# Kernel optimization log

Hardware: AMD Instinct MI355X
Metric: run time of the kernel (lower is better)

Reference implementation:

```python
import jax, jax.numpy as jnp
import numpy as np

EMBED = 1024
HEADS = 16
HEAD_DIM = EMBED // HEADS


def setup_inputs() -> dict:
    key = jax.random.key(0)
    ks = jax.random.split(key, 9)
    s = 0.02
    x = jax.random.normal(ks[0], (2, 2048, EMBED), dtype=jnp.float32)
    Wq = jax.random.normal(ks[1], (EMBED, EMBED), dtype=jnp.float32) * s
    bq = jnp.zeros((EMBED,), dtype=jnp.float32)
    Wk = jax.random.normal(ks[2], (EMBED, EMBED), dtype=jnp.float32) * s
    bk = jnp.zeros((EMBED,), dtype=jnp.float32)
    Wv = jax.random.normal(ks[3], (EMBED, EMBED), dtype=jnp.float32) * s
    bv = jnp.zeros((EMBED,), dtype=jnp.float32)
    Wo = jax.random.normal(ks[4], (EMBED, EMBED), dtype=jnp.float32) * s
    bo = jnp.zeros((EMBED,), dtype=jnp.float32)
    return {"x": x, "Wq": Wq, "bq": bq, "Wk": Wk, "bk": bk,
            "Wv": Wv, "bv": bv, "Wo": Wo, "bo": bo}


def reference(x, Wq, bq, Wk, bk, Wv, bv, Wo, bo):
    B, S, E = x.shape
    H, D = HEADS, HEAD_DIM
    scale = jnp.sqrt(jnp.asarray(D, dtype=x.dtype))
    # projections (torch Linear: y = x @ W.T + b)
    q = (x @ Wq.T + bq).reshape(B, S, H, D).transpose(0, 2, 1, 3)  # [B,H,S,D]
    k = (x @ Wk.T + bk).reshape(B, S, H, D).transpose(0, 2, 1, 3)
    v = (x @ Wv.T + bv).reshape(B, S, H, D).transpose(0, 2, 1, 3)
    scores = jnp.einsum('bhqd,bhkd->bhqk', q, k) / scale  # [B,H,S,S]
    probs = jax.nn.softmax(scores, axis=-1)
    out = jnp.einsum('bhqk,bhkd->bhqd', probs, v)  # [B,H,S,D]
    out = out.transpose(0, 2, 1, 3).reshape(B, S, E)
    return out @ Wo.T + bo
```

## Files before the change

### kernel.cpp

```cpp
#include <hip/hip_runtime.h>
#include <cstddef>

#define EMBED 1024
#define HEADS 16
#define HDIM  64
#define BATCH 2
#define SEQ   2048
#define MTOT  (BATCH*SEQ)

typedef __attribute__((ext_vector_type(8)))  short short8;
typedef __attribute__((ext_vector_type(4)))  float f32x4;
typedef __attribute__((ext_vector_type(16))) float f32x16;

typedef __attribute__((address_space(1))) const unsigned int* gas_u32p;
typedef __attribute__((address_space(3))) unsigned int* las_u32p;

static __device__ __forceinline__ void gload_lds16(const void* g, void* l) {
    __builtin_amdgcn_global_load_lds((gas_u32p)g, (las_u32p)l, 16, 0, 0);
}

static __device__ __forceinline__ unsigned short f2bf(float x) {
    unsigned u = __builtin_bit_cast(unsigned, x);
    unsigned r = (u + 0x7FFFu + ((u >> 16) & 1u)) >> 16;
    return (unsigned short)r;
}

static __device__ __forceinline__ unsigned pk_bf16(float lo, float hi) {
    unsigned r;
    asm("v_cvt_pk_bf16_f32 %0, %1, %2" : "=v"(r) : "v"(lo), "v"(hi));
    return r;
}

static __device__ __forceinline__ void plane32_swap(unsigned &a, unsigned &b) {
    auto r = __builtin_amdgcn_permlane32_swap((int)a, (int)b, false, false);
    a = (unsigned)r[0];
    b = (unsigned)r[1];
}

static __device__ __forceinline__ f32x16 mfma32(short8 a, short8 b, f32x16 c) {
    return __builtin_amdgcn_mfma_f32_32x32x16_bf16(a, b, c, 0, 0, 0);
}

__global__ __launch_bounds__(256)
void convx(const float* __restrict__ x, unsigned short* __restrict__ xh)
{
    const size_t i = ((size_t)blockIdx.x * 256 + threadIdx.x) * 8;
    float4 a = *(const float4*)(x + i);
    float4 b = *(const float4*)(x + i + 4);
    unsigned short o[8] __attribute__((aligned(16)));
    o[0] = f2bf(a.x); o[1] = f2bf(a.y); o[2] = f2bf(a.z); o[3] = f2bf(a.w);
    o[4] = f2bf(b.x); o[5] = f2bf(b.y); o[6] = f2bf(b.z); o[7] = f2bf(b.w);
    *(uint4*)(xh + i) = *(const uint4*)o;
}

__global__ __launch_bounds__(256)
void convw(const float* __restrict__ Wq, const float* __restrict__ Wk,
           const float* __restrict__ Wv, const float* __restrict__ Wo,
           unsigned short* __restrict__ Wh)
{
    const int sel = blockIdx.y;
    const float* src = sel == 0 ? Wq : sel == 1 ? Wk : sel == 2 ? Wv : Wo;
    unsigned short* dst = Wh + (size_t)sel * EMBED * EMBED;
    const size_t i = ((size_t)blockIdx.x * 256 + threadIdx.x) * 4;
    float4 a = *(const float4*)(src + i);
    ushort4 o;
    o.x = f2bf(a.x); o.y = f2bf(a.y); o.z = f2bf(a.z); o.w = f2bf(a.w);
    *(ushort4*)(dst + i) = o;
}

__global__ __launch_bounds__(256)
void gemm_qkv_bf16(const unsigned short* __restrict__ A,
                   const unsigned short* __restrict__ Wqh,
                   const unsigned short* __restrict__ Wkh,
                   const unsigned short* __restrict__ Wvh,
                   const float* __restrict__ bq,
                   const float* __restrict__ bk,
                   const float* __restrict__ bv,
                   unsigned short* __restrict__ Qb,
                   unsigned short* __restrict__ Kb,
                   unsigned short* __restrict__ Vt)
{
    __shared__ short As[128 * 32];
    __shared__ short Bs[128 * 32];

    const int tid  = threadIdx.x;
    const int lane = tid & 63;
    const int w    = tid >> 6;
    const int c    = lane & 15;
    const int g    = lane >> 4;
    const int wr   = w >> 1;
    const int wc   = w & 1;

    const int m0   = blockIdx.y * 128;
    const int bx   = blockIdx.x;
    const int wsel = bx >> 3;
    const int n0   = (bx & 7) * 128;

    const unsigned short* W = (wsel == 0) ? Wqh : (wsel == 1) ? Wkh : Wvh;
    const float* bias       = (wsel == 0) ? bq  : (wsel == 1) ? bk  : bv;

    f32x4 acc[4][4] = {};

    for (int k0 = 0; k0 < EMBED; k0 += 32) {
        __syncthreads();
        #pragma unroll
        for (int i = 0; i < 2; ++i) {
            int s   = (w * 2 + i) * 64 + lane;
            int row = s >> 2;
            int k8  = (s & 3) * 8;
            gload_lds16(A + (size_t)(m0 + row) * EMBED + k0 + k8,
                        As + (size_t)(w * 2 + i) * 512);
            gload_lds16(W + (size_t)(n0 + row) * EMBED + k0 + k8,
                        Bs + (size_t)(w * 2 + i) * 512);
        }
        __syncthreads();

        short8 af[4], bf[4];
        #pragma unroll
        for (int mi = 0; mi < 4; ++mi)
            af[mi] = *(const short8*)&As[(wr * 64 + mi * 16 + c) * 32 + g * 8];
        #pragma unroll
        for (int ni = 0; ni < 4; ++ni)
            bf[ni] = *(const short8*)&Bs[(wc * 64 + ni * 16 + c) * 32 + g * 8];
        #pragma unroll
        for (int mi = 0; mi < 4; ++mi)
            #pragma unroll
            for (int ni = 0; ni < 4; ++ni)
                acc[mi][ni] = __builtin_amdgcn_mfma_f32_16x16x32_bf16(
                    af[mi], bf[ni], acc[mi][ni], 0, 0, 0);
    }

    if (wsel == 2) {
        #pragma unroll
        for (int mi = 0; mi < 4; ++mi) {
            const int m  = m0 + wr * 64 + mi * 16 + g * 4;
            const int bb = m >> 11;
            const int ss = m & (SEQ - 1);
            #pragma unroll
            for (int ni = 0; ni < 4; ++ni) {
                const int col = n0 + wc * 64 + ni * 16 + c;
                const int hh = col >> 6, dd = col & 63;
                const float bi_ = bias[col];
                ushort4 o;
                o.x = f2bf(acc[mi][ni][0] + bi_);
                o.y = f2bf(acc[mi][ni][1] + bi_);
                o.z = f2bf(acc[mi][ni][2] + bi_);
                o.w = f2bf(acc[mi][ni][3] + bi_);
                *(ushort4*)&Vt[((size_t)((bb * HEADS + hh) * HDIM) + dd) * SEQ + ss] = o;
            }
        }
    } else {
        unsigned short* Out = (wsel == 0) ? Qb : Kb;
        const float oscale  = (wsel == 0) ? 0.180336880f : 1.0f;
        #pragma unroll
        for (int mi = 0; mi < 4; ++mi)
            #pragma unroll
            for (int r = 0; r < 4; ++r) {
                const int m = m0 + wr * 64 + mi * 16 + g * 4 + r;
                #pragma unroll
                for (int ni = 0; ni < 4; ++ni) {
                    const int col = n0 + wc * 64 + ni * 16 + c;
                    Out[(size_t)m * EMBED + col] =
                        f2bf((acc[mi][ni][r] + bias[col]) * oscale);
                }
            }
    }
}

__global__ __launch_bounds__(256)
void gemm_o_bf16(const unsigned short* __restrict__ A,
                 const unsigned short* __restrict__ Woh,
                 const float* __restrict__ bo,
                 float* __restrict__ C)
{
    __shared__ short As[128 * 32];
    __shared__ short Bs[128 * 32];

    const int tid  = threadIdx.x;
    const int lane = tid & 63;
    const int w    = tid >> 6;
    const int c    = lane & 15;
    const int g    = lane >> 4;
    const int wr   = w >> 1;
    const int wc   = w & 1;

    const int m0 = blockIdx.y * 128;
    const int n0 = blockIdx.x * 128;

    f32x4 acc[4][4] = {};

    for (int k0 = 0; k0 < EMBED; k0 += 32) {
        __syncthreads();
        #pragma unroll
        for (int i = 0; i < 2; ++i) {
            int s   = (w * 2 + i) * 64 + lane;
            int row = s >> 2;
            int k8  = (s & 3) * 8;
            gload_lds16(A + (size_t)(m0 + row) * EMBED + k0 + k8,
                        As + (size_t)(w * 2 + i) * 512);
            gload_lds16(Woh + (size_t)(n0 + row) * EMBED + k0 + k8,
                        Bs + (size_t)(w * 2 + i) * 512);
        }
        __syncthreads();

        short8 af[4], bf[4];
        #pragma unroll
        for (int mi = 0; mi < 4; ++mi)
            af[mi] = *(const short8*)&As[(wr * 64 + mi * 16 + c) * 32 + g * 8];
        #pragma unroll
        for (int ni = 0; ni < 4; ++ni)
            bf[ni] = *(const short8*)&Bs[(wc * 64 + ni * 16 + c) * 32 + g * 8];
        #pragma unroll
        for (int mi = 0; mi < 4; ++mi)
            #pragma unroll
            for (int ni = 0; ni < 4; ++ni)
                acc[mi][ni] = __builtin_amdgcn_mfma_f32_16x16x32_bf16(
                    af[mi], bf[ni], acc[mi][ni], 0, 0, 0);
    }

    #pragma unroll
    for (int mi = 0; mi < 4; ++mi)
        #pragma unroll
        for (int r = 0; r < 4; ++r) {
            const int m = m0 + wr * 64 + mi * 16 + g * 4 + r;
            #pragma unroll
            for (int ni = 0; ni < 4; ++ni) {
                const int col = n0 + wc * 64 + ni * 16 + c;
                C[(size_t)m * EMBED + col] = acc[mi][ni][r] + bo[col];
            }
        }
}

__global__ __launch_bounds__(512, 4)
void flash_attn_mfma5(const unsigned short* __restrict__ Qb,
                      const unsigned short* __restrict__ Kb,
                      const unsigned short* __restrict__ Vt,
                      unsigned short* __restrict__ O)
{
    __shared__ short KT[2][2][64 * 64];
    __shared__ short VT[2][2][64 * 64];

    const int tid  = threadIdx.x;
    const int lane = tid & 63;
    const int w    = tid >> 6;
    const int qt   = w & 3;
    const int half = w >> 2;
    const int l31  = lane & 31;
    const int hi   = lane >> 5;
    const int q0   = blockIdx.x * 128 + qt * 32;
    const int h    = blockIdx.y;
    const int b    = blockIdx.z;

    short8 qf[4];
    {
        const unsigned short* qrow =
            Qb + (size_t)(b * SEQ + q0 + l31) * EMBED + h * HDIM + hi * 8;
        #pragma unroll
        for (int kc = 0; kc < 4; ++kc)
            qf[kc] = *(const short8*)(qrow + kc * 16);
    }

    const int tb     = w >> 1;
    const int sthalf = tb >> 1;
    const int stV    = tb & 1;
    const int ssub   = w & 1;
    const int strow  = ssub * 32 + (lane >> 3);
    const int ch     = (lane & 7) ^ (strow & 7);
    const unsigned short* kS =
        Kb + (size_t)(b * SEQ + sthalf * (SEQ / 2) + strow) * EMBED + h * HDIM + ch * 8;
    const unsigned short* vS =
        Vt + ((size_t)((b * HEADS + h) * HDIM) + strow) * SEQ + sthalf * (SEQ / 2) + ch * 8;

    f32x16 acc[2] = {};
    float l_run = 0.f;

    #define STAGE(kt2, bb)                                                    \
        do {                                                                  \
            if (stV == 0) {                                                   \
                const unsigned short* src = kS + (size_t)(kt2) * 64 * EMBED;  \
                short* kd = &KT[sthalf][bb][ssub * 2048];                     \
                _Pragma("unroll")                                             \
                for (int it = 0; it < 4; ++it)                                \
                    gload_lds16(src + (size_t)it * 8 * EMBED, kd + it * 512); \
            } else {                                                          \
                const unsigned short* src = vS + (kt2) * 64;                  \
                short* vd = &VT[sthalf][bb][ssub * 2048];                     \
                _Pragma("unroll")                                             \
                for (int it = 0; it < 4; ++it)                                \
                    gload_lds16(src + (size_t)it * 8 * SEQ, vd + it * 512);   \
            }                                                                 \
        } while (0)

    STAGE(0, 0);
    __syncthreads();

    for (int kt = 0; kt < SEQ / 2 / 64; ++kt) {
        const int bi = kt & 1;
        if (kt < SEQ / 2 / 64 - 1) STAGE(kt + 1, bi ^ 1);

        const short* kb_ = &KT[half][bi][0];
        const short* vb_ = &VT[half][bi][0];

        f32x16 s[2] = {};
        __builtin_amdgcn_s_setprio(1);
        #pragma unroll
        for (int t = 0; t < 2; ++t) {
            const int row = t * 32 + l31;
            const int rm  = l31 & 7;
            #pragma unroll
            for (int kc = 0; kc < 4; ++kc) {
                short8 ka = *(const short8*)&kb_[row * 64 + (((2 * kc + hi) ^ rm) * 8)];
                s[t] = mfma32(ka, qf[kc], s[t]);
            }
        }
        __builtin_amdgcn_s_setprio(0);

        float rs = 0.f;
        #pragma unroll
        for (int t = 0; t < 2; ++t)
            #pragma unroll
            for (int r = 0; r < 16; ++r) {
                float pv = __builtin_amdgcn_exp2f(s[t][r]);
                s[t][r] = pv;
                rs += pv;
            }
        rs += __shfl_xor(rs, 32, 64);
        l_run += rs;

        short8 pf[2][2];
        #pragma unroll
        for (int t = 0; t < 2; ++t)
            #pragma unroll
            for (int kc = 0; kc < 2; ++kc) {
                unsigned A0 = pk_bf16(s[t][8 * kc + 0], s[t][8 * kc + 1]);
                unsigned A1 = pk_bf16(s[t][8 * kc + 2], s[t][8 * kc + 3]);
                unsigned B0 = pk_bf16(s[t][8 * kc + 4], s[t][8 * kc + 5]);
                unsigned B1 = pk_bf16(s[t][8 * kc + 6], s[t][8 * kc + 7]);
                plane32_swap(A0, B0);
                plane32_swap(A1, B1);
                uint4 fw = make_uint4(A0, A1, B0, B1);
                pf[t][kc] = __builtin_bit_cast(short8, fw);
            }

        __builtin_amdgcn_s_setprio(1);
        #pragma unroll
        for (int dt = 0; dt < 2; ++dt) {
            const int row = dt * 32 + l31;
            const int rm  = l31 & 7;
            #pragma unroll
            for (int t = 0; t < 2; ++t)
                #pragma unroll
                for (int kc = 0; kc < 2; ++kc) {
                    short8 vf = *(const short8*)
                        &vb_[row * 64 + (((4 * t + 2 * kc + hi) ^ rm) * 8)];
                    acc[dt] = mfma32(pf[t][kc], vf, acc[dt]);
                }
        }
        __builtin_amdgcn_s_setprio(0);

        __syncthreads();
    }
    #undef STAGE

    float* mrgf = (float*)&KT[0][0][0];
    float* mlbf = (float*)&VT[0][0][0];
    if (half == 1) {
        #pragma unroll
        for (int dt = 0; dt < 2; ++dt)
            #pragma unroll
            for (int r = 0; r < 16; ++r) {
                const int qr = (r & 3) + 8 * (r >> 2) + 4 * hi;
                mrgf[qt * 2048 + qr * 64 + dt * 32 + l31] = acc[dt][r];
            }
        if (lane < 32)
            mlbf[qt * 32 + lane] = l_run;
    }
    __syncthreads();
    if (half == 0) {
        const float lo  = mlbf[qt * 32 + l31];
        const float inv = 1.f / (l_run + lo);
        #pragma unroll
        for (int r = 0; r < 16; ++r) {
            const int qr = (r & 3) + 8 * (r >> 2) + 4 * hi;
            float invr = __shfl(inv, qr, 64);
            #pragma unroll
            for (int dt = 0; dt < 2; ++dt) {
                float oh  = mrgf[qt * 2048 + qr * 64 + dt * 32 + l31];
                float val = (acc[dt][r] + oh) * invr;
                O[(size_t)(b * SEQ + q0 + qr) * EMBED + h * HDIM + dt * 32 + l31]
                    = f2bf(val);
            }
        }
    }
}

extern "C" void kernel_launch(void* const* d_in, const int* in_sizes, int n_in,
                              void* d_out, int out_size, void* d_ws, size_t ws_size,
                              hipStream_t stream)
{
    const float* x  = (const float*)d_in[0];
    const float* Wq = (const float*)d_in[1];
    const float* bq = (const float*)d_in[2];
    const float* Wk = (const float*)d_in[3];
    const float* bk = (const float*)d_in[4];
    const float* Wv = (const float*)d_in[5];
    const float* bv = (const float*)d_in[6];
    const float* Wo = (const float*)d_in[7];
    const float* bo = (const float*)d_in[8];
    float* out = (float*)d_out;

    const size_t ME = (size_t)MTOT * EMBED;
    unsigned short* xh   = (unsigned short*)d_ws;
    unsigned short* Qb   = xh   + ME;
    unsigned short* Kb   = Qb   + ME;
    unsigned short* Vt   = Kb   + ME;
    unsigned short* attn = Vt   + ME;
    unsigned short* Wh   = attn + ME;

    dim3 blk(256);

    convx<<<dim3(MTOT * EMBED / 2048), blk, 0, stream>>>(x, xh);
    convw<<<dim3(EMBED * EMBED / 1024, 4), blk, 0, stream>>>(Wq, Wk, Wv, Wo, Wh);

    gemm_qkv_bf16<<<dim3(24, MTOT / 128), blk, 0, stream>>>(
        xh, Wh, Wh + (size_t)EMBED * EMBED, Wh + 2 * (size_t)EMBED * EMBED,
        bq, bk, bv, Qb, Kb, Vt);

    flash_attn_mfma5<<<dim3(SEQ / 128, HEADS, BATCH), dim3(512), 0, stream>>>(
        Qb, Kb, Vt, attn);

    gemm_o_bf16<<<dim3(EMBED / 128, MTOT / 128), blk, 0, stream>>>(
        attn, Wh + 3 * (size_t)EMBED * EMBED, bo, out);
}
```

Baseline: 125.9 us.

## Double-buffer LDS in projection GEMMs and remap blocks for XCD locality

```diff
diff --git a/kernel.cpp b/kernel.cpp
--- a/kernel.cpp
+++ b/kernel.cpp
@@ -80,8 +80,8 @@
                    unsigned short* __restrict__ Kb,
                    unsigned short* __restrict__ Vt)
 {
-    __shared__ short As[128 * 32];
-    __shared__ short Bs[128 * 32];
+    __shared__ short As[2][128 * 32];
+    __shared__ short Bs[2][128 * 32];
 
     const int tid  = threadIdx.x;
     const int lane = tid & 63;
@@ -91,44 +91,61 @@
     const int wr   = w >> 1;
     const int wc   = w & 1;
 
-    const int m0   = blockIdx.y * 128;
-    const int bx   = blockIdx.x;
-    const int wsel = bx >> 3;
-    const int n0   = (bx & 7) * 128;
+    const int lg   = (blockIdx.x & 7) * 96 + (blockIdx.x >> 3);
+    const int m0   = (lg / 24) * 128;
+    const int bxn  = lg % 24;
+    const int wsel = bxn >> 3;
+    const int n0   = (bxn & 7) * 128;
 
     const unsigned short* W = (wsel == 0) ? Wqh : (wsel == 1) ? Wkh : Wvh;
     const float* bias       = (wsel == 0) ? bq  : (wsel == 1) ? bk  : bv;
 
+    const int srow = (w * 2) * 16 + (lane >> 2);
+    const int sk8  = (lane & 3) * 8;
+    const unsigned short* aS0 = A + (size_t)(m0 + srow) * EMBED + sk8;
+    const unsigned short* aS1 = A + (size_t)(m0 + srow + 16) * EMBED + sk8;
+    const unsigned short* bS0 = W + (size_t)(n0 + srow) * EMBED + sk8;
+    const unsigned short* bS1 = W + (size_t)(n0 + srow + 16) * EMBED + sk8;
+    const int d0 = (w * 2) * 512;
+    const int d1 = (w * 2 + 1) * 512;
+
+    #define GSTAGE(bb)                                 \
+        do {                                           \
+            gload_lds16(aS0, &As[bb][d0]);             \
+            gload_lds16(aS1, &As[bb][d1]);             \
+            gload_lds16(bS0, &Bs[bb][d0]);             \
+            gload_lds16(bS1, &Bs[bb][d1]);             \
+            aS0 += 32; aS1 += 32; bS0 += 32; bS1 += 32;\
+        } while (0)
+
     f32x4 acc[4][4] = {};
 
-    for (int k0 = 0; k0 < EMBED; k0 += 32) {
-        __syncthreads();
-        #pragma unroll
-        for (int i = 0; i < 2; ++i) {
-            int s   = (w * 2 + i) * 64 + lane;
-            int row = s >> 2;
-            int k8  = (s & 3) * 8;
-            gload_lds16(A + (size_t)(m0 + row) * EMBED + k0 + k8,
-                        As + (size_t)(w * 2 + i) * 512);
-            gload_lds16(W + (size_t)(n0 + row) * EMBED + k0 + k8,
-                        Bs + (size_t)(w * 2 + i) * 512);
-        }
-        __syncthreads();
+    GSTAGE(0);
+    __syncthreads();
+
+    for (int t = 0; t < EMBED / 32; ++t) {
+        const int cb = t & 1;
+        if (t < EMBED / 32 - 1) GSTAGE(cb ^ 1);
 
         short8 af[4], bf[4];
         #pragma unroll
         for (int mi = 0; mi < 4; ++mi)
-            af[mi] = *(const short8*)&As[(wr * 64 + mi * 16 + c) * 32 + g * 8];
+            af[mi] = *(const short8*)&As[cb][(wr * 64 + mi * 16 + c) * 32 + g * 8];
         #pragma unroll
         for (int ni = 0; ni < 4; ++ni)
-            bf[ni] = *(const short8*)&Bs[(wc * 64 + ni * 16 + c) * 32 + g * 8];
+            bf[ni] = *(const short8*)&Bs[cb][(wc * 64 + ni * 16 + c) * 32 + g * 8];
+        __builtin_amdgcn_s_setprio(1);
         #pragma unroll
         for (int mi = 0; mi < 4; ++mi)
             #pragma unroll
             for (int ni = 0; ni < 4; ++ni)
                 acc[mi][ni] = __builtin_amdgcn_mfma_f32_16x16x32_bf16(
                     af[mi], bf[ni], acc[mi][ni], 0, 0, 0);
-    }
+        __builtin_amdgcn_s_setprio(0);
+
+        __syncthreads();
+    }
+    #undef GSTAGE
 
     if (wsel == 2) {
         #pragma unroll
@@ -173,8 +190,8 @@
                  const float* __restrict__ bo,
                  float* __restrict__ C)
 {
-    __shared__ short As[128 * 32];
-    __shared__ short Bs[128 * 32];
+    __shared__ short As[2][128 * 32];
+    __shared__ short Bs[2][128 * 32];
 
     const int tid  = threadIdx.x;
     const int lane = tid & 63;
@@ -184,39 +201,56 @@
     const int wr   = w >> 1;
     const int wc   = w & 1;
 
-    const int m0 = blockIdx.y * 128;
-    const int n0 = blockIdx.x * 128;
+    const int lg = (blockIdx.x & 7) * 32 + (blockIdx.x >> 3);
+    const int m0 = (lg >> 3) * 128;
+    const int n0 = (lg & 7) * 128;
+
+    const int srow = (w * 2) * 16 + (lane >> 2);
+    const int sk8  = (lane & 3) * 8;
+    const unsigned short* aS0 = A   + (size_t)(m0 + srow) * EMBED + sk8;
+    const unsigned short* aS1 = A   + (size_t)(m0 + srow + 16) * EMBED + sk8;
+    const unsigned short* bS0 = Woh + (size_t)(n0 + srow) * EMBED + sk8;
+    const unsigned short* bS1 = Woh + (size_t)(n0 + srow + 16) * EMBED + sk8;
+    const int d0 = (w * 2) * 512;
+    const int d1 = (w * 2 + 1) * 512;
+
+    #define GSTAGE(bb)                                 \
+        do {                                           \
+            gload_lds16(aS0, &As[bb][d0]);             \
+            gload_lds16(aS1, &As[bb][d1]);             \
+            gload_lds16(bS0, &Bs[bb][d0]);             \
+            gload_lds16(bS1, &Bs[bb][d1]);             \
+            aS0 += 32; aS1 += 32; bS0 += 32; bS1 += 32;\
+        } while (0)
 
     f32x4 acc[4][4] = {};
 
-    for (int k0 = 0; k0 < EMBED; k0 += 32) {
-        __syncthreads();
-        #pragma unroll
-        for (int i = 0; i < 2; ++i) {
-            int s   = (w * 2 + i) * 64 + lane;
-            int row = s >> 2;
-            int k8  = (s & 3) * 8;
-            gload_lds16(A + (size_t)(m0 + row) * EMBED + k0 + k8,
-                        As + (size_t)(w * 2 + i) * 512);
-            gload_lds16(Woh + (size_t)(n0 + row) * EMBED + k0 + k8,
-                        Bs + (size_t)(w * 2 + i) * 512);
-        }
-        __syncthreads();
+    GSTAGE(0);
+    __syncthreads();
+
+    for (int t = 0; t < EMBED / 32; ++t) {
+        const int cb = t & 1;
+        if (t < EMBED / 32 - 1) GSTAGE(cb ^ 1);
 
         short8 af[4], bf[4];
         #pragma unroll
         for (int mi = 0; mi < 4; ++mi)
-            af[mi] = *(const short8*)&As[(wr * 64 + mi * 16 + c) * 32 + g * 8];
+            af[mi] = *(const short8*)&As[cb][(wr * 64 + mi * 16 + c) * 32 + g * 8];
         #pragma unroll
         for (int ni = 0; ni < 4; ++ni)
-            bf[ni] = *(const short8*)&Bs[(wc * 64 + ni * 16 + c) * 32 + g * 8];
+            bf[ni] = *(const short8*)&Bs[cb][(wc * 64 + ni * 16 + c) * 32 + g * 8];
+        __builtin_amdgcn_s_setprio(1);
         #pragma unroll
         for (int mi = 0; mi < 4; ++mi)
             #pragma unroll
             for (int ni = 0; ni < 4; ++ni)
                 acc[mi][ni] = __builtin_amdgcn_mfma_f32_16x16x32_bf16(
                     af[mi], bf[ni], acc[mi][ni], 0, 0, 0);
-    }
+        __builtin_amdgcn_s_setprio(0);
+
+        __syncthreads();
+    }
+    #undef GSTAGE
 
     #pragma unroll
     for (int mi = 0; mi < 4; ++mi)
@@ -422,13 +456,13 @@
     convx<<<dim3(MTOT * EMBED / 2048), blk, 0, stream>>>(x, xh);
     convw<<<dim3(EMBED * EMBED / 1024, 4), blk, 0, stream>>>(Wq, Wk, Wv, Wo, Wh);
 
-    gemm_qkv_bf16<<<dim3(24, MTOT / 128), blk, 0, stream>>>(
+    gemm_qkv_bf16<<<dim3(768), blk, 0, stream>>>(
         xh, Wh, Wh + (size_t)EMBED * EMBED, Wh + 2 * (size_t)EMBED * EMBED,
         bq, bk, bv, Qb, Kb, Vt);
 
     flash_attn_mfma5<<<dim3(SEQ / 128, HEADS, BATCH), dim3(512), 0, stream>>>(
         Qb, Kb, Vt, attn);
 
-    gemm_o_bf16<<<dim3(EMBED / 128, MTOT / 128), blk, 0, stream>>>(
+    gemm_o_bf16<<<dim3(256), blk, 0, stream>>>(
         attn, Wh + 3 * (size_t)EMBED * EMBED, bo, out);
 }
```

Result: slower. 137.2 us (+9.0%).

## Rewrite QKV GEMM with 256x256 tiles, double-buffered swizzled LDS, phased MFMA

Applied to the files above, without the earlier changes.

```diff
diff --git a/kernel.cpp b/kernel.cpp
--- a/kernel.cpp
+++ b/kernel.cpp
@@ -68,102 +68,150 @@
     *(ushort4*)(dst + i) = o;
 }
 
-__global__ __launch_bounds__(256)
-void gemm_qkv_bf16(const unsigned short* __restrict__ A,
-                   const unsigned short* __restrict__ Wqh,
-                   const unsigned short* __restrict__ Wkh,
-                   const unsigned short* __restrict__ Wvh,
-                   const float* __restrict__ bq,
-                   const float* __restrict__ bk,
-                   const float* __restrict__ bv,
-                   unsigned short* __restrict__ Qb,
-                   unsigned short* __restrict__ Kb,
-                   unsigned short* __restrict__ Vt)
-{
-    __shared__ short As[128 * 32];
-    __shared__ short Bs[128 * 32];
+__global__ __launch_bounds__(512, 2)
+void gemm_qkv_8ph(const unsigned short* __restrict__ A,
+                  const unsigned short* __restrict__ Wqh,
+                  const unsigned short* __restrict__ Wkh,
+                  const unsigned short* __restrict__ Wvh,
+                  const float* __restrict__ bq,
+                  const float* __restrict__ bk,
+                  const float* __restrict__ bv,
+                  unsigned short* __restrict__ Qb,
+                  unsigned short* __restrict__ Kb,
+                  unsigned short* __restrict__ Vt)
+{
+    __shared__ short AL[2][256 * 64];
+    __shared__ short BL[2][256 * 64];
 
     const int tid  = threadIdx.x;
     const int lane = tid & 63;
     const int w    = tid >> 6;
+    const int wm   = w >> 2;
+    const int wn   = w & 3;
     const int c    = lane & 15;
     const int g    = lane >> 4;
-    const int wr   = w >> 1;
-    const int wc   = w & 1;
-
-    const int m0   = blockIdx.y * 128;
+
+    const int m0   = blockIdx.y * 256;
     const int bx   = blockIdx.x;
-    const int wsel = bx >> 3;
-    const int n0   = (bx & 7) * 128;
+    const int wsel = bx >> 2;
+    const int n0   = (bx & 3) * 256;
 
     const unsigned short* W = (wsel == 0) ? Wqh : (wsel == 1) ? Wkh : Wvh;
     const float* bias       = (wsel == 0) ? bq  : (wsel == 1) ? bk  : bv;
 
-    f32x4 acc[4][4] = {};
-
-    for (int k0 = 0; k0 < EMBED; k0 += 32) {
-        __syncthreads();
-        #pragma unroll
-        for (int i = 0; i < 2; ++i) {
-            int s   = (w * 2 + i) * 64 + lane;
-            int row = s >> 2;
-            int k8  = (s & 3) * 8;
-            gload_lds16(A + (size_t)(m0 + row) * EMBED + k0 + k8,
-                        As + (size_t)(w * 2 + i) * 512);
-            gload_lds16(W + (size_t)(n0 + row) * EMBED + k0 + k8,
-                        Bs + (size_t)(w * 2 + i) * 512);
-        }
-        __syncthreads();
-
-        short8 af[4], bf[4];
-        #pragma unroll
-        for (int mi = 0; mi < 4; ++mi)
-            af[mi] = *(const short8*)&As[(wr * 64 + mi * 16 + c) * 32 + g * 8];
-        #pragma unroll
-        for (int ni = 0; ni < 4; ++ni)
-            bf[ni] = *(const short8*)&Bs[(wc * 64 + ni * 16 + c) * 32 + g * 8];
-        #pragma unroll
-        for (int mi = 0; mi < 4; ++mi)
-            #pragma unroll
-            for (int ni = 0; ni < 4; ++ni)
-                acc[mi][ni] = __builtin_amdgcn_mfma_f32_16x16x32_bf16(
-                    af[mi], bf[ni], acc[mi][ni], 0, 0, 0);
-    }
+    const int s0  = tid;
+    const int s1  = 512 + tid;
+    const int r0  = s0 >> 3;
+    const int r1  = s1 >> 3;
+    const int cs0 = (s0 & 7) ^ (r0 & 7);
+    const int cs1 = (s1 & 7) ^ (r1 & 7);
+    const int db0 = (0 * 512 + w * 64) * 8;
+    const int db1 = (1 * 512 + w * 64) * 8;
+
+    #define STG(bb, p, kofs)                                                   \
+        do {                                                                   \
+            const unsigned short* gbase = ((p) < 2) ? A : W;                   \
+            const int mn0 = ((p) < 2) ? m0 : n0;                               \
+            short* ldsb = ((p) < 2) ? &AL[bb][0] : &BL[bb][0];                 \
+            const int hf = (p) & 1;                                           \
+            gload_lds16(gbase + (size_t)(mn0 + hf * 128 + r0) * EMBED          \
+                              + (kofs) + cs0 * 8,                             \
+                        ldsb + hf * 8192 + db0);                              \
+            gload_lds16(gbase + (size_t)(mn0 + hf * 128 + r1) * EMBED          \
+                              + (kofs) + cs1 * 8,                             \
+                        ldsb + hf * 8192 + db1);                              \
+        } while (0)
+
+    f32x4 acc[4][4][2] = {};
+
+    STG(0, 0, 0); STG(0, 1, 0); STG(0, 2, 0); STG(0, 3, 0);
+    asm volatile("s_waitcnt vmcnt(0)" ::: "memory");
+    __builtin_amdgcn_s_barrier();
+
+    for (int i = 0; i < 16; ++i) {
+        const int pi = i & 1;
+        const int kn = (i + 1) * 64;
+        #pragma unroll
+        for (int p = 0; p < 4; ++p) {
+            if (i < 15) STG(pi ^ 1, p, kn);
+
+            const short* Ab = &AL[pi][0];
+            const short* Bb = &BL[pi][0];
+            short8 af[2][4], bf[2][2];
+            #pragma unroll
+            for (int ks = 0; ks < 2; ++ks) {
+                #pragma unroll
+                for (int mi = 0; mi < 4; ++mi) {
+                    const int row = wm * 128 + (p >> 1) * 64 + mi * 16 + c;
+                    const int chn = (ks * 4 + g) ^ (c & 7);
+                    af[ks][mi] = *(const short8*)&Ab[row * 64 + chn * 8];
+                }
+                #pragma unroll
+                for (int ni = 0; ni < 2; ++ni) {
+                    const int row = wn * 64 + (p & 1) * 32 + ni * 16 + c;
+                    const int chn = (ks * 4 + g) ^ (c & 7);
+                    bf[ks][ni] = *(const short8*)&Bb[row * 64 + chn * 8];
+                }
+            }
+
+            __builtin_amdgcn_s_barrier();
+
+            __builtin_amdgcn_s_setprio(1);
+            #pragma unroll
+            for (int mi = 0; mi < 4; ++mi)
+                #pragma unroll
+                for (int ni = 0; ni < 2; ++ni)
+                    #pragma unroll
+                    for (int ks = 0; ks < 2; ++ks)
+                        acc[p][mi][ni] = __builtin_amdgcn_mfma_f32_16x16x32_bf16(
+                            af[ks][mi], bf[ks][ni], acc[p][mi][ni], 0, 0, 0);
+            __builtin_amdgcn_s_setprio(0);
+
+            if (p == 3)
+                asm volatile("s_waitcnt vmcnt(0)" ::: "memory");
+            __builtin_amdgcn_s_barrier();
+        }
+    }
+    #undef STG
 
     if (wsel == 2) {
         #pragma unroll
-        for (int mi = 0; mi < 4; ++mi) {
-            const int m  = m0 + wr * 64 + mi * 16 + g * 4;
-            const int bb = m >> 11;
-            const int ss = m & (SEQ - 1);
-            #pragma unroll
-            for (int ni = 0; ni < 4; ++ni) {
-                const int col = n0 + wc * 64 + ni * 16 + c;
-                const int hh = col >> 6, dd = col & 63;
-                const float bi_ = bias[col];
-                ushort4 o;
-                o.x = f2bf(acc[mi][ni][0] + bi_);
-                o.y = f2bf(acc[mi][ni][1] + bi_);
-                o.z = f2bf(acc[mi][ni][2] + bi_);
-                o.w = f2bf(acc[mi][ni][3] + bi_);
-                *(ushort4*)&Vt[((size_t)((bb * HEADS + hh) * HDIM) + dd) * SEQ + ss] = o;
-            }
-        }
+        for (int p = 0; p < 4; ++p)
+            #pragma unroll
+            for (int mi = 0; mi < 4; ++mi) {
+                const int m  = m0 + wm * 128 + (p >> 1) * 64 + mi * 16 + g * 4;
+                const int bb = m >> 11;
+                const int ss = m & (SEQ - 1);
+                #pragma unroll
+                for (int ni = 0; ni < 2; ++ni) {
+                    const int col = n0 + wn * 64 + (p & 1) * 32 + ni * 16 + c;
+                    const int hh = col >> 6, dd = col & 63;
+                    const float bi_ = bias[col];
+                    ushort4 o;
+                    o.x = f2bf(acc[p][mi][ni][0] + bi_);
+                    o.y = f2bf(acc[p][mi][ni][1] + bi_);
+                    o.z = f2bf(acc[p][mi][ni][2] + bi_);
+                    o.w = f2bf(acc[p][mi][ni][3] + bi_);
+                    *(ushort4*)&Vt[((size_t)((bb * HEADS + hh) * HDIM) + dd) * SEQ + ss] = o;
+                }
+            }
     } else {
         unsigned short* Out = (wsel == 0) ? Qb : Kb;
         const float oscale  = (wsel == 0) ? 0.180336880f : 1.0f;
         #pragma unroll
-        for (int mi = 0; mi < 4; ++mi)
-            #pragma unroll
-            for (int r = 0; r < 4; ++r) {
-                const int m = m0 + wr * 64 + mi * 16 + g * 4 + r;
-                #pragma unroll
-                for (int ni = 0; ni < 4; ++ni) {
-                    const int col = n0 + wc * 64 + ni * 16 + c;
-                    Out[(size_t)m * EMBED + col] =
-                        f2bf((acc[mi][ni][r] + bias[col]) * oscale);
+        for (int p = 0; p < 4; ++p)
+            #pragma unroll
+            for (int mi = 0; mi < 4; ++mi)
+                #pragma unroll
+                for (int r = 0; r < 4; ++r) {
+                    const int m = m0 + wm * 128 + (p >> 1) * 64 + mi * 16 + g * 4 + r;
+                    #pragma unroll
+                    for (int ni = 0; ni < 2; ++ni) {
+                        const int col = n0 + wn * 64 + (p & 1) * 32 + ni * 16 + c;
+                        Out[(size_t)m * EMBED + col] =
+                            f2bf((acc[p][mi][ni][r] + bias[col]) * oscale);
+                    }
                 }
-            }
     }
 }
 
@@ -210,12 +258,14 @@
         #pragma unroll
         for (int ni = 0; ni < 4; ++ni)
             bf[ni] = *(const short8*)&Bs[(wc * 64 + ni * 16 + c) * 32 + g * 8];
+        __builtin_amdgcn_s_setprio(1);
         #pragma unroll
         for (int mi = 0; mi < 4; ++mi)
             #pragma unroll
             for (int ni = 0; ni < 4; ++ni)
                 acc[mi][ni] = __builtin_amdgcn_mfma_f32_16x16x32_bf16(
                     af[mi], bf[ni], acc[mi][ni], 0, 0, 0);
+        __builtin_amdgcn_s_setprio(0);
     }
 
     #pragma unroll
@@ -422,7 +472,7 @@
     convx<<<dim3(MTOT * EMBED / 2048), blk, 0, stream>>>(x, xh);
     convw<<<dim3(EMBED * EMBED / 1024, 4), blk, 0, stream>>>(Wq, Wk, Wv, Wo, Wh);
 
-    gemm_qkv_bf16<<<dim3(24, MTOT / 128), blk, 0, stream>>>(
+    gemm_qkv_8ph<<<dim3(12, MTOT / 256), dim3(512), 0, stream>>>(
         xh, Wh, Wh + (size_t)EMBED * EMBED, Wh + 2 * (size_t)EMBED * EMBED,
         bq, bk, bv, Qb, Kb, Vt);
 
```

Measured after the change: 136.9 us. 1.09x slower.

## Double-buffer LDS tiles in QKV GEMM and raise MFMA wave priority

Applied to the files above, without the earlier changes.

```diff
diff --git a/kernel.cpp b/kernel.cpp
--- a/kernel.cpp
+++ b/kernel.cpp
@@ -80,8 +80,8 @@
                    unsigned short* __restrict__ Kb,
                    unsigned short* __restrict__ Vt)
 {
-    __shared__ short As[128 * 32];
-    __shared__ short Bs[128 * 32];
+    __shared__ short As[2][128 * 32];
+    __shared__ short Bs[2][128 * 32];
 
     const int tid  = threadIdx.x;
     const int lane = tid & 63;
@@ -92,43 +92,59 @@
     const int wc   = w & 1;
 
     const int m0   = blockIdx.y * 128;
-    const int bx   = blockIdx.x;
-    const int wsel = bx >> 3;
-    const int n0   = (bx & 7) * 128;
+    const int bxn  = blockIdx.x;
+    const int wsel = bxn >> 3;
+    const int n0   = (bxn & 7) * 128;
 
     const unsigned short* W = (wsel == 0) ? Wqh : (wsel == 1) ? Wkh : Wvh;
     const float* bias       = (wsel == 0) ? bq  : (wsel == 1) ? bk  : bv;
 
+    const int srow = (w * 2) * 16 + (lane >> 2);
+    const int sk8  = (lane & 3) * 8;
+    const unsigned short* aS0 = A + (size_t)(m0 + srow) * EMBED + sk8;
+    const unsigned short* aS1 = A + (size_t)(m0 + srow + 16) * EMBED + sk8;
+    const unsigned short* bS0 = W + (size_t)(n0 + srow) * EMBED + sk8;
+    const unsigned short* bS1 = W + (size_t)(n0 + srow + 16) * EMBED + sk8;
+    const int d0 = (w * 2) * 512;
+    const int d1 = (w * 2 + 1) * 512;
+
+    #define GSTAGE(bb)                                 \
+        do {                                           \
+            gload_lds16(aS0, &As[bb][d0]);             \
+            gload_lds16(aS1, &As[bb][d1]);             \
+            gload_lds16(bS0, &Bs[bb][d0]);             \
+            gload_lds16(bS1, &Bs[bb][d1]);             \
+            aS0 += 32; aS1 += 32; bS0 += 32; bS1 += 32;\
+        } while (0)
+
     f32x4 acc[4][4] = {};
 
-    for (int k0 = 0; k0 < EMBED; k0 += 32) {
-        __syncthreads();
-        #pragma unroll
-        for (int i = 0; i < 2; ++i) {
-            int s   = (w * 2 + i) * 64 + lane;
-            int row = s >> 2;
-            int k8  = (s & 3) * 8;
-            gload_lds16(A + (size_t)(m0 + row) * EMBED + k0 + k8,
-                        As + (size_t)(w * 2 + i) * 512);
-            gload_lds16(W + (size_t)(n0 + row) * EMBED + k0 + k8,
-                        Bs + (size_t)(w * 2 + i) * 512);
-        }
-        __syncthreads();
+    GSTAGE(0);
+    __syncthreads();
+
+    for (int t = 0; t < EMBED / 32; ++t) {
+        const int cb = t & 1;
+        if (t < EMBED / 32 - 1) GSTAGE(cb ^ 1);
 
         short8 af[4], bf[4];
         #pragma unroll
         for (int mi = 0; mi < 4; ++mi)
-            af[mi] = *(const short8*)&As[(wr * 64 + mi * 16 + c) * 32 + g * 8];
+            af[mi] = *(const short8*)&As[cb][(wr * 64 + mi * 16 + c) * 32 + g * 8];
         #pragma unroll
         for (int ni = 0; ni < 4; ++ni)
-            bf[ni] = *(const short8*)&Bs[(wc * 64 + ni * 16 + c) * 32 + g * 8];
+            bf[ni] = *(const short8*)&Bs[cb][(wc * 64 + ni * 16 + c) * 32 + g * 8];
+        __builtin_amdgcn_s_setprio(1);
         #pragma unroll
         for (int mi = 0; mi < 4; ++mi)
             #pragma unroll
             for (int ni = 0; ni < 4; ++ni)
                 acc[mi][ni] = __builtin_amdgcn_mfma_f32_16x16x32_bf16(
                     af[mi], bf[ni], acc[mi][ni], 0, 0, 0);
-    }
+        __builtin_amdgcn_s_setprio(0);
+
+        __syncthreads();
+    }
+    #undef GSTAGE
 
     if (wsel == 2) {
         #pragma unroll
@@ -210,12 +226,14 @@
         #pragma unroll
         for (int ni = 0; ni < 4; ++ni)
             bf[ni] = *(const short8*)&Bs[(wc * 64 + ni * 16 + c) * 32 + g * 8];
+        __builtin_amdgcn_s_setprio(1);
         #pragma unroll
         for (int mi = 0; mi < 4; ++mi)
             #pragma unroll
             for (int ni = 0; ni < 4; ++ni)
                 acc[mi][ni] = __builtin_amdgcn_mfma_f32_16x16x32_bf16(
                     af[mi], bf[ni], acc[mi][ni], 0, 0, 0);
+        __builtin_amdgcn_s_setprio(0);
     }
 
     #pragma unroll
```

New measurement: 134.1 us. 6.5% more time.
